# Performance work log

Hardware: AMD Instinct MI355X
Metric: run time of the kernel (lower is better)

The kernel has to match this reference:

```python
import jax, jax.numpy as jnp
import numpy as np
import math

S = 8192
D = 1024


def setup_inputs() -> dict:
    key = jax.random.key(0)
    kq, kk, kv = jax.random.split(key, 3)
    q = jax.random.normal(kq, (S, D), dtype=jnp.float32)
    k = jax.random.normal(kk, (S, D), dtype=jnp.float32)
    v = jax.random.normal(kv, (S, D), dtype=jnp.float32)
    return {"q": q, "k": k, "v": v}


def reference(q, k, v):
    # att[s_q, s_k] = q . k  (contract over d), scaled by 1/sqrt(d_model)
    d_model = q.shape[-1]
    scale = 1.0 / math.sqrt(d_model)
    att = jnp.einsum('qd,kd->qk', q, k) * scale
    # Original module applies its manual max-stable softmax over dim=1,
    # which for this rank-2 score matrix is the key axis (last axis).
    att_score = jax.nn.softmax(att, axis=1)
    return jnp.einsum('qk,kd->qd', att_score, v)
```

## Files before the change

### kernel.cpp

```cpp
#include <hip/hip_runtime.h>
#include <hip/hip_bf16.h>

#define S 8192
#define D 1024
#define QBLK 32
#define NW 8
#define KVBLK 256
#define NITER (S/KVBLK)
#define NTHR (NW*64)

typedef short short8 __attribute__((ext_vector_type(8)));
typedef float f32x16 __attribute__((ext_vector_type(16)));

__device__ __forceinline__ unsigned short f2bf(float x) {
    unsigned u = __builtin_bit_cast(unsigned, x);
    u += 0x7FFFu + ((u >> 16) & 1u);
    return (unsigned short)(u >> 16);
}
__device__ __forceinline__ float fexp2(float x) { return __builtin_amdgcn_exp2f(x); }

__device__ __forceinline__ short8 lds_r16(const char* rowbase, int off, int swz) {
    uint2 a = *(const uint2*)(rowbase + (off ^ swz));
    uint2 b = *(const uint2*)(rowbase + ((off + 8) ^ swz));
    int4 w; w.x = (int)a.x; w.y = (int)a.y; w.z = (int)b.x; w.w = (int)b.y;
    return __builtin_bit_cast(short8, w);
}
__device__ __forceinline__ void lds_w16(char* rowbase, int off, int swz, short8 v) {
    int4 w = __builtin_bit_cast(int4, v);
    uint2 a; a.x = (unsigned)w.x; a.y = (unsigned)w.y;
    uint2 b; b.x = (unsigned)w.z; b.y = (unsigned)w.w;
    *(uint2*)(rowbase + (off ^ swz))       = a;
    *(uint2*)(rowbase + ((off + 8) ^ swz)) = b;
}

__global__ void pack_k_kernel(const float* __restrict__ in, unsigned short* __restrict__ out) {
    int idx  = blockIdx.x * 256 + threadIdx.x;
    int lane = idx & 63, dc = (idx >> 6) & 63, kt = idx >> 12;
    int row = kt * 32 + (lane & 31), col = dc * 16 + (lane >> 5) * 8;
    const float4* p = (const float4*)(in + (size_t)row * D + col);
    float4 a = p[0], b = p[1];
    short8 v;
    v[0] = (short)f2bf(a.x); v[1] = (short)f2bf(a.y); v[2] = (short)f2bf(a.z); v[3] = (short)f2bf(a.w);
    v[4] = (short)f2bf(b.x); v[5] = (short)f2bf(b.y); v[6] = (short)f2bf(b.z); v[7] = (short)f2bf(b.w);
    *(short8*)(out + (size_t)idx * 8) = v;
}

__global__ void pack_v_kernel(const float* __restrict__ in, unsigned short* __restrict__ out) {
    int idx  = blockIdx.x * 256 + threadIdx.x;
    int lane = idx & 63, db = (idx >> 6) & 31, kc = (idx >> 11) & 15, t = idx >> 15;
    int col = db * 32 + (lane & 31);
    int rowbase = t * 256 + kc * 16 + (lane >> 5) * 8;
    short8 v;
#pragma unroll
    for (int j = 0; j < 8; ++j)
        v[j] = (short)f2bf(in[(size_t)(rowbase + j) * D + col]);
    *(short8*)(out + (size_t)idx * 8) = v;
}

template<bool CONV>
__global__ __launch_bounds__(NTHR, 2)
void attn_kernel(const float* __restrict__ Qf,
                 const unsigned short* __restrict__ Kpk,
                 const unsigned short* __restrict__ Vpk,
                 const float* __restrict__ Kf,
                 const float* __restrict__ Vf,
                 float* __restrict__ Out)
{
    __shared__ unsigned short q_lds[QBLK * D];
    __shared__ unsigned short p_lds[QBLK * KVBLK];
    __shared__ float red_m[NW][QBLK];
    __shared__ float red_l[NW][QBLK];
    __shared__ float alpha_sh[QBLK];
    __shared__ float invl_sh[QBLK];

    const int tid  = threadIdx.x;
    const int wid  = tid >> 6;
    const int lane = tid & 63;
    const int ln31 = lane & 31;
    const int hi   = (lane >> 5) & 1;
    const int q0   = blockIdx.x * QBLK;
    const int swz  = (ln31 & 15) << 3;

    {
        const float cscale = 1.44269504088896340736f / 32.0f;
        const float* qg = Qf + (size_t)q0 * D;
        char* qb = (char*)q_lds;
#pragma unroll
        for (int it = 0; it < (QBLK * D) / (NTHR * 8); ++it) {
            int idx = (it * NTHR + tid) * 8;
            int qq = idx >> 10, dd = idx & (D - 1);
            const float4* p4 = (const float4*)(qg + idx);
            float4 a = p4[0], b = p4[1];
            short8 v;
            v[0] = (short)f2bf(a.x * cscale); v[1] = (short)f2bf(a.y * cscale);
            v[2] = (short)f2bf(a.z * cscale); v[3] = (short)f2bf(a.w * cscale);
            v[4] = (short)f2bf(b.x * cscale); v[5] = (short)f2bf(b.y * cscale);
            v[6] = (short)f2bf(b.z * cscale); v[7] = (short)f2bf(b.w * cscale);
            lds_w16(qb + qq * 2048, dd * 2, (qq & 15) << 3, v);
        }
    }

    f32x16 O0, O1, O2, O3;
#pragma unroll
    for (int i = 0; i < 16; ++i) { O0[i] = 0.f; O1[i] = 0.f; O2[i] = 0.f; O3[i] = 0.f; }
    float m_run = -1e30f, l_run = 0.f;

    __syncthreads();

    for (int t = 0; t < NITER; ++t) {
        f32x16 s0, s1;
#pragma unroll
        for (int i = 0; i < 16; ++i) { s0[i] = 0.f; s1[i] = 0.f; }

        const char* qb = (const char*)q_lds + ln31 * 2048;
        __builtin_amdgcn_s_setprio(1);
        if (CONV) {
            const unsigned short* kg = Kpk + ((size_t)(t * 8 + wid) * 4096 + lane) * 8;
#pragma unroll 8
            for (int dc = 0; dc < 64; dc += 2) {
                short8 a0 = *(const short8*)(kg + (size_t)dc * 512);
                short8 b0 = lds_r16(qb, dc * 32 + hi * 16, swz);
                s0 = __builtin_amdgcn_mfma_f32_32x32x16_bf16(a0, b0, s0, 0, 0, 0);
                short8 a1 = *(const short8*)(kg + (size_t)(dc + 1) * 512);
                short8 b1 = lds_r16(qb, (dc + 1) * 32 + hi * 16, swz);
                s1 = __builtin_amdgcn_mfma_f32_32x32x16_bf16(a1, b1, s1, 0, 0, 0);
            }
        } else {
            const int krow = t * KVBLK + wid * 32 + ln31;
            const float* kg = Kf + (size_t)krow * D + hi * 8;
#pragma unroll 2
            for (int dc = 0; dc < 64; ++dc) {
                const float4* f4 = (const float4*)(kg + dc * 16);
                float4 x = f4[0], y = f4[1];
                short8 a0;
                a0[0] = (short)f2bf(x.x); a0[1] = (short)f2bf(x.y); a0[2] = (short)f2bf(x.z); a0[3] = (short)f2bf(x.w);
                a0[4] = (short)f2bf(y.x); a0[5] = (short)f2bf(y.y); a0[6] = (short)f2bf(y.z); a0[7] = (short)f2bf(y.w);
                short8 b0 = lds_r16(qb, dc * 32 + hi * 16, swz);
                s0 = __builtin_amdgcn_mfma_f32_32x32x16_bf16(a0, b0, s0, 0, 0, 0);
            }
        }
        __builtin_amdgcn_s_setprio(0);
#pragma unroll
        for (int i = 0; i < 16; ++i) s0[i] += s1[i];

        float mloc = s0[0];
#pragma unroll
        for (int r = 1; r < 16; ++r) mloc = fmaxf(mloc, s0[r]);
        mloc = fmaxf(mloc, __shfl_xor(mloc, 32));
        if (lane < 32) red_m[wid][ln31] = mloc;
        __syncthreads();

        float mt = red_m[0][ln31];
#pragma unroll
        for (int w = 1; w < NW; ++w) mt = fmaxf(mt, red_m[w][ln31]);
        float mnew  = fmaxf(m_run, mt);
        float alpha = fexp2(m_run - mnew);

        float pr[16];
        float lloc = 0.f;
#pragma unroll
        for (int r = 0; r < 16; ++r) { pr[r] = fexp2(s0[r] - mnew); lloc += pr[r]; }
        lloc += __shfl_xor(lloc, 32);
        if (lane < 32) { red_l[wid][ln31] = lloc; if (wid == 0) alpha_sh[ln31] = alpha; }

        {
            char* pb = (char*)p_lds + ln31 * 512;
#pragma unroll
            for (int g = 0; g < 4; ++g) {
                unsigned p01 = (unsigned)f2bf(pr[4 * g + 0]) | ((unsigned)f2bf(pr[4 * g + 1]) << 16);
                unsigned p23 = (unsigned)f2bf(pr[4 * g + 2]) | ((unsigned)f2bf(pr[4 * g + 3]) << 16);
                uint2 val = make_uint2(p01, p23);
                int koff = (wid * 32 + 8 * g + 4 * hi) * 2;
                *(uint2*)(pb + (koff ^ swz)) = val;
            }
        }
        __syncthreads();

        float lsum = red_l[0][ln31];
#pragma unroll
        for (int w = 1; w < NW; ++w) lsum += red_l[w][ln31];
        l_run = l_run * alpha + lsum;
        m_run = mnew;

#pragma unroll
        for (int r = 0; r < 16; ++r) {
            float ar = alpha_sh[(r & 3) + 8 * (r >> 2) + 4 * hi];
            O0[r] *= ar; O1[r] *= ar; O2[r] *= ar; O3[r] *= ar;
        }

        const char* pbase = (const char*)p_lds + ln31 * 512;
        __builtin_amdgcn_s_setprio(1);
        if (CONV) {
            const unsigned short* vg = Vpk + ((size_t)(t * 16) * 2048 + (size_t)wid * 64 + lane) * 8;
#pragma unroll 4
            for (int kc = 0; kc < 16; ++kc) {
                short8 pa = lds_r16(pbase, kc * 32 + hi * 16, swz);
                const unsigned short* vk = vg + (size_t)kc * 16384;
                short8 v0 = *(const short8*)(vk);
                O0 = __builtin_amdgcn_mfma_f32_32x32x16_bf16(pa, v0, O0, 0, 0, 0);
                short8 v1 = *(const short8*)(vk + 4096);
                O1 = __builtin_amdgcn_mfma_f32_32x32x16_bf16(pa, v1, O1, 0, 0, 0);
                short8 v2 = *(const short8*)(vk + 8192);
                O2 = __builtin_amdgcn_mfma_f32_32x32x16_bf16(pa, v2, O2, 0, 0, 0);
                short8 v3 = *(const short8*)(vk + 12288);
                O3 = __builtin_amdgcn_mfma_f32_32x32x16_bf16(pa, v3, O3, 0, 0, 0);
            }
        } else {
            const int dcol0 = wid * 32 + ln31;
#pragma unroll 2
            for (int kc = 0; kc < 16; ++kc) {
                short8 pa = lds_r16(pbase, kc * 32 + hi * 16, swz);
                const float* vf = Vf + (size_t)(t * 256 + kc * 16 + hi * 8) * D + dcol0;
#pragma unroll
                for (int f = 0; f < 4; ++f) {
                    short8 vb;
#pragma unroll
                    for (int j = 0; j < 8; ++j)
                        vb[j] = (short)f2bf(vf[(size_t)j * D + f * 256]);
                    if (f == 0) O0 = __builtin_amdgcn_mfma_f32_32x32x16_bf16(pa, vb, O0, 0, 0, 0);
                    if (f == 1) O1 = __builtin_amdgcn_mfma_f32_32x32x16_bf16(pa, vb, O1, 0, 0, 0);
                    if (f == 2) O2 = __builtin_amdgcn_mfma_f32_32x32x16_bf16(pa, vb, O2, 0, 0, 0);
                    if (f == 3) O3 = __builtin_amdgcn_mfma_f32_32x32x16_bf16(pa, vb, O3, 0, 0, 0);
                }
            }
        }
        __builtin_amdgcn_s_setprio(0);
    }

    if (wid == 0 && lane < 32) invl_sh[ln31] = 1.0f / l_run;
    __syncthreads();

    float* outp = Out + (size_t)q0 * D + wid * 32 + ln31;
#pragma unroll
    for (int r = 0; r < 16; ++r) {
        int qrow = (r & 3) + 8 * (r >> 2) + 4 * hi;
        float inv = invl_sh[qrow];
        outp[(size_t)qrow * D + 0]   = O0[r] * inv;
        outp[(size_t)qrow * D + 256] = O1[r] * inv;
        outp[(size_t)qrow * D + 512] = O2[r] * inv;
        outp[(size_t)qrow * D + 768] = O3[r] * inv;
    }
}

extern "C" void kernel_launch(void* const* d_in, const int* in_sizes, int n_in,
                              void* d_out, int out_size, void* d_ws, size_t ws_size,
                              hipStream_t stream)
{
    const float* q = (const float*)d_in[0];
    const float* k = (const float*)d_in[1];
    const float* v = (const float*)d_in[2];
    float* out = (float*)d_out;

    const size_t need = (size_t)2 * S * D * sizeof(unsigned short);
    if (ws_size >= need) {
        unsigned short* kpk = (unsigned short*)d_ws;
        unsigned short* vpk = kpk + (size_t)S * D;
        hipLaunchKernelGGL(pack_k_kernel, dim3(S * D / (256 * 8)), dim3(256), 0, stream, k, kpk);
        hipLaunchKernelGGL(pack_v_kernel, dim3(S * D / (256 * 8)), dim3(256), 0, stream, v, vpk);
        hipLaunchKernelGGL((attn_kernel<true>), dim3(S / QBLK), dim3(NTHR), 0, stream,
                           q, kpk, vpk, (const float*)nullptr, (const float*)nullptr, out);
    } else {
        hipLaunchKernelGGL((attn_kernel<false>), dim3(S / QBLK), dim3(NTHR), 0, stream,
                           q, (const unsigned short*)nullptr, (const unsigned short*)nullptr, k, v, out);
    }
}
```

Measured before the change: 633.5 us.

## Software-pipeline QK^T of next tile with PV of current tile

```diff
diff --git a/kernel.cpp b/kernel.cpp
--- a/kernel.cpp
+++ b/kernel.cpp
@@ -57,17 +57,53 @@
     *(short8*)(out + (size_t)idx * 8) = v;
 }
 
-template<bool CONV>
+#define SOFTMAX_PHASE(BUF)                                                        \
+    {                                                                             \
+        _Pragma("unroll")                                                         \
+        for (int i = 0; i < 16; ++i) s0[i] += s1[i];                              \
+        float mloc = s0[0];                                                       \
+        _Pragma("unroll")                                                         \
+        for (int r = 1; r < 16; ++r) mloc = fmaxf(mloc, s0[r]);                   \
+        mloc = fmaxf(mloc, __shfl_xor(mloc, 32));                                 \
+        if (lane < 32) red_m[wid][ln31] = mloc;                                   \
+        __syncthreads();                                                          \
+        float mt = red_m[0][ln31];                                                \
+        _Pragma("unroll")                                                         \
+        for (int w = 1; w < NW; ++w) mt = fmaxf(mt, red_m[w][ln31]);              \
+        float mnew  = fmaxf(m_run, mt);                                           \
+        float alpha = fexp2(m_run - mnew);                                        \
+        float pr[16]; float lloc = 0.f;                                           \
+        _Pragma("unroll")                                                         \
+        for (int r = 0; r < 16; ++r) { pr[r] = fexp2(s0[r] - mnew); lloc += pr[r]; } \
+        lloc += __shfl_xor(lloc, 32);                                             \
+        if (lane < 32) { red_l[wid][ln31] = lloc; if (wid == 0) alpha_sh[ln31] = alpha; } \
+        {                                                                         \
+            char* pb = (char*)(&p_lds[BUF][0]) + ln31 * 512;                      \
+            _Pragma("unroll")                                                     \
+            for (int g = 0; g < 4; ++g) {                                         \
+                unsigned p01 = (unsigned)f2bf(pr[4*g+0]) | ((unsigned)f2bf(pr[4*g+1]) << 16); \
+                unsigned p23 = (unsigned)f2bf(pr[4*g+2]) | ((unsigned)f2bf(pr[4*g+3]) << 16); \
+                uint2 val = make_uint2(p01, p23);                                 \
+                int koff = (wid * 32 + 8 * g + 4 * hi) * 2;                       \
+                *(uint2*)(pb + (koff ^ swz)) = val;                               \
+            }                                                                     \
+        }                                                                         \
+        __syncthreads();                                                          \
+        float lsum = red_l[0][ln31];                                              \
+        _Pragma("unroll")                                                         \
+        for (int w = 1; w < NW; ++w) lsum += red_l[w][ln31];                      \
+        l_run = l_run * alpha + lsum;                                             \
+        m_run = mnew;                                                             \
+    }
+
 __global__ __launch_bounds__(NTHR, 2)
-void attn_kernel(const float* __restrict__ Qf,
-                 const unsigned short* __restrict__ Kpk,
-                 const unsigned short* __restrict__ Vpk,
-                 const float* __restrict__ Kf,
-                 const float* __restrict__ Vf,
-                 float* __restrict__ Out)
+void attn_pipe_kernel(const float* __restrict__ Qf,
+                      const unsigned short* __restrict__ Kpk,
+                      const unsigned short* __restrict__ Vpk,
+                      float* __restrict__ Out)
 {
     __shared__ unsigned short q_lds[QBLK * D];
-    __shared__ unsigned short p_lds[QBLK * KVBLK];
+    __shared__ unsigned short p_lds[2][QBLK * KVBLK];
     __shared__ float red_m[NW][QBLK];
     __shared__ float red_l[NW][QBLK];
     __shared__ float alpha_sh[QBLK];
@@ -84,7 +120,7 @@
     {
         const float cscale = 1.44269504088896340736f / 32.0f;
         const float* qg = Qf + (size_t)q0 * D;
-        char* qb = (char*)q_lds;
+        char* qbw = (char*)q_lds;
 #pragma unroll
         for (int it = 0; it < (QBLK * D) / (NTHR * 8); ++it) {
             int idx = (it * NTHR + tid) * 8;
@@ -96,135 +132,189 @@
             v[2] = (short)f2bf(a.z * cscale); v[3] = (short)f2bf(a.w * cscale);
             v[4] = (short)f2bf(b.x * cscale); v[5] = (short)f2bf(b.y * cscale);
             v[6] = (short)f2bf(b.z * cscale); v[7] = (short)f2bf(b.w * cscale);
-            lds_w16(qb + qq * 2048, dd * 2, (qq & 15) << 3, v);
-        }
-    }
-
-    f32x16 O0, O1, O2, O3;
+            lds_w16(qbw + qq * 2048, dd * 2, (qq & 15) << 3, v);
+        }
+    }
+
+    f32x16 O0, O1, O2, O3, s0, s1;
 #pragma unroll
     for (int i = 0; i < 16; ++i) { O0[i] = 0.f; O1[i] = 0.f; O2[i] = 0.f; O3[i] = 0.f; }
     float m_run = -1e30f, l_run = 0.f;
 
     __syncthreads();
 
+    const char* qb = (const char*)q_lds + ln31 * 2048;
+
+    {
+#pragma unroll
+        for (int i = 0; i < 16; ++i) { s0[i] = 0.f; s1[i] = 0.f; }
+        const unsigned short* kg = Kpk + ((size_t)(0 * 8 + wid) * 4096 + lane) * 8;
+        __builtin_amdgcn_s_setprio(1);
+#pragma unroll 8
+        for (int dc = 0; dc < 64; dc += 2) {
+            short8 a0 = *(const short8*)(kg + (size_t)dc * 512);
+            short8 b0 = lds_r16(qb, dc * 32 + hi * 16, swz);
+            s0 = __builtin_amdgcn_mfma_f32_32x32x16_bf16(a0, b0, s0, 0, 0, 0);
+            short8 a1 = *(const short8*)(kg + (size_t)(dc + 1) * 512);
+            short8 b1 = lds_r16(qb, (dc + 1) * 32 + hi * 16, swz);
+            s1 = __builtin_amdgcn_mfma_f32_32x32x16_bf16(a1, b1, s1, 0, 0, 0);
+        }
+        __builtin_amdgcn_s_setprio(0);
+    }
+    SOFTMAX_PHASE(0)
+
+    int cur = 0;
     for (int t = 0; t < NITER; ++t) {
-        f32x16 s0, s1;
-#pragma unroll
-        for (int i = 0; i < 16; ++i) { s0[i] = 0.f; s1[i] = 0.f; }
-
-        const char* qb = (const char*)q_lds + ln31 * 2048;
-        __builtin_amdgcn_s_setprio(1);
-        if (CONV) {
-            const unsigned short* kg = Kpk + ((size_t)(t * 8 + wid) * 4096 + lane) * 8;
-#pragma unroll 8
-            for (int dc = 0; dc < 64; dc += 2) {
-                short8 a0 = *(const short8*)(kg + (size_t)dc * 512);
-                short8 b0 = lds_r16(qb, dc * 32 + hi * 16, swz);
-                s0 = __builtin_amdgcn_mfma_f32_32x32x16_bf16(a0, b0, s0, 0, 0, 0);
-                short8 a1 = *(const short8*)(kg + (size_t)(dc + 1) * 512);
-                short8 b1 = lds_r16(qb, (dc + 1) * 32 + hi * 16, swz);
-                s1 = __builtin_amdgcn_mfma_f32_32x32x16_bf16(a1, b1, s1, 0, 0, 0);
-            }
-        } else {
-            const int krow = t * KVBLK + wid * 32 + ln31;
-            const float* kg = Kf + (size_t)krow * D + hi * 8;
-#pragma unroll 2
-            for (int dc = 0; dc < 64; ++dc) {
-                const float4* f4 = (const float4*)(kg + dc * 16);
-                float4 x = f4[0], y = f4[1];
-                short8 a0;
-                a0[0] = (short)f2bf(x.x); a0[1] = (short)f2bf(x.y); a0[2] = (short)f2bf(x.z); a0[3] = (short)f2bf(x.w);
-                a0[4] = (short)f2bf(y.x); a0[5] = (short)f2bf(y.y); a0[6] = (short)f2bf(y.z); a0[7] = (short)f2bf(y.w);
-                short8 b0 = lds_r16(qb, dc * 32 + hi * 16, swz);
-                s0 = __builtin_amdgcn_mfma_f32_32x32x16_bf16(a0, b0, s0, 0, 0, 0);
-            }
-        }
-        __builtin_amdgcn_s_setprio(0);
-#pragma unroll
-        for (int i = 0; i < 16; ++i) s0[i] += s1[i];
-
-        float mloc = s0[0];
-#pragma unroll
-        for (int r = 1; r < 16; ++r) mloc = fmaxf(mloc, s0[r]);
-        mloc = fmaxf(mloc, __shfl_xor(mloc, 32));
-        if (lane < 32) red_m[wid][ln31] = mloc;
-        __syncthreads();
-
-        float mt = red_m[0][ln31];
-#pragma unroll
-        for (int w = 1; w < NW; ++w) mt = fmaxf(mt, red_m[w][ln31]);
-        float mnew  = fmaxf(m_run, mt);
-        float alpha = fexp2(m_run - mnew);
-
-        float pr[16];
-        float lloc = 0.f;
-#pragma unroll
-        for (int r = 0; r < 16; ++r) { pr[r] = fexp2(s0[r] - mnew); lloc += pr[r]; }
-        lloc += __shfl_xor(lloc, 32);
-        if (lane < 32) { red_l[wid][ln31] = lloc; if (wid == 0) alpha_sh[ln31] = alpha; }
-
-        {
-            char* pb = (char*)p_lds + ln31 * 512;
-#pragma unroll
-            for (int g = 0; g < 4; ++g) {
-                unsigned p01 = (unsigned)f2bf(pr[4 * g + 0]) | ((unsigned)f2bf(pr[4 * g + 1]) << 16);
-                unsigned p23 = (unsigned)f2bf(pr[4 * g + 2]) | ((unsigned)f2bf(pr[4 * g + 3]) << 16);
-                uint2 val = make_uint2(p01, p23);
-                int koff = (wid * 32 + 8 * g + 4 * hi) * 2;
-                *(uint2*)(pb + (koff ^ swz)) = val;
-            }
-        }
-        __syncthreads();
-
-        float lsum = red_l[0][ln31];
-#pragma unroll
-        for (int w = 1; w < NW; ++w) lsum += red_l[w][ln31];
-        l_run = l_run * alpha + lsum;
-        m_run = mnew;
-
 #pragma unroll
         for (int r = 0; r < 16; ++r) {
             float ar = alpha_sh[(r & 3) + 8 * (r >> 2) + 4 * hi];
             O0[r] *= ar; O1[r] *= ar; O2[r] *= ar; O3[r] *= ar;
         }
-
-        const char* pbase = (const char*)p_lds + ln31 * 512;
+        const char* pbase = (const char*)(&p_lds[cur][0]) + ln31 * 512;
+        const unsigned short* vg = Vpk + ((size_t)(t * 16) * 2048 + (size_t)wid * 64 + lane) * 8;
+
         __builtin_amdgcn_s_setprio(1);
-        if (CONV) {
-            const unsigned short* vg = Vpk + ((size_t)(t * 16) * 2048 + (size_t)wid * 64 + lane) * 8;
+        if (t + 1 < NITER) {
+#pragma unroll
+            for (int i = 0; i < 16; ++i) { s0[i] = 0.f; s1[i] = 0.f; }
+            const unsigned short* kg = Kpk + ((size_t)((t + 1) * 8 + wid) * 4096 + lane) * 8;
+            short8 pa{};
+#pragma unroll 8
+            for (int i = 0; i < 64; ++i) {
+                const int kc = i >> 2, f = i & 3;
+                if (f == 0) pa = lds_r16(pbase, kc * 32 + hi * 16, swz);
+                short8 ak = *(const short8*)(kg + (size_t)i * 512);
+                short8 bq = lds_r16(qb, i * 32 + hi * 16, swz);
+                if (i & 1) s1 = __builtin_amdgcn_mfma_f32_32x32x16_bf16(ak, bq, s1, 0, 0, 0);
+                else       s0 = __builtin_amdgcn_mfma_f32_32x32x16_bf16(ak, bq, s0, 0, 0, 0);
+                short8 vv = *(const short8*)(vg + (size_t)kc * 16384 + (size_t)f * 4096);
+                if      (f == 0) O0 = __builtin_amdgcn_mfma_f32_32x32x16_bf16(pa, vv, O0, 0, 0, 0);
+                else if (f == 1) O1 = __builtin_amdgcn_mfma_f32_32x32x16_bf16(pa, vv, O1, 0, 0, 0);
+                else if (f == 2) O2 = __builtin_amdgcn_mfma_f32_32x32x16_bf16(pa, vv, O2, 0, 0, 0);
+                else             O3 = __builtin_amdgcn_mfma_f32_32x32x16_bf16(pa, vv, O3, 0, 0, 0);
+            }
+        } else {
 #pragma unroll 4
             for (int kc = 0; kc < 16; ++kc) {
                 short8 pa = lds_r16(pbase, kc * 32 + hi * 16, swz);
                 const unsigned short* vk = vg + (size_t)kc * 16384;
-                short8 v0 = *(const short8*)(vk);
-                O0 = __builtin_amdgcn_mfma_f32_32x32x16_bf16(pa, v0, O0, 0, 0, 0);
-                short8 v1 = *(const short8*)(vk + 4096);
-                O1 = __builtin_amdgcn_mfma_f32_32x32x16_bf16(pa, v1, O1, 0, 0, 0);
-                short8 v2 = *(const short8*)(vk + 8192);
-                O2 = __builtin_amdgcn_mfma_f32_32x32x16_bf16(pa, v2, O2, 0, 0, 0);
-                short8 v3 = *(const short8*)(vk + 12288);
-                O3 = __builtin_amdgcn_mfma_f32_32x32x16_bf16(pa, v3, O3, 0, 0, 0);
+                O0 = __builtin_amdgcn_mfma_f32_32x32x16_bf16(pa, *(const short8*)(vk),         O0, 0, 0, 0);
+                O1 = __builtin_amdgcn_mfma_f32_32x32x16_bf16(pa, *(const short8*)(vk + 4096),  O1, 0, 0, 0);
+                O2 = __builtin_amdgcn_mfma_f32_32x32x16_bf16(pa, *(const short8*)(vk + 8192),  O2, 0, 0, 0);
+                O3 = __builtin_amdgcn_mfma_f32_32x32x16_bf16(pa, *(const short8*)(vk + 12288), O3, 0, 0, 0);
             }
-        } else {
-            const int dcol0 = wid * 32 + ln31;
+        }
+        __builtin_amdgcn_s_setprio(0);
+
+        if (t + 1 < NITER) {
+            if (cur == 0) { SOFTMAX_PHASE(1) } else { SOFTMAX_PHASE(0) }
+        }
+        cur ^= 1;
+    }
+
+    if (wid == 0 && lane < 32) invl_sh[ln31] = 1.0f / l_run;
+    __syncthreads();
+
+    float* outp = Out + (size_t)q0 * D + wid * 32 + ln31;
+#pragma unroll
+    for (int r = 0; r < 16; ++r) {
+        int qrow = (r & 3) + 8 * (r >> 2) + 4 * hi;
+        float inv = invl_sh[qrow];
+        outp[(size_t)qrow * D + 0]   = O0[r] * inv;
+        outp[(size_t)qrow * D + 256] = O1[r] * inv;
+        outp[(size_t)qrow * D + 512] = O2[r] * inv;
+        outp[(size_t)qrow * D + 768] = O3[r] * inv;
+    }
+}
+
+__global__ __launch_bounds__(NTHR, 2)
+void attn_fallback_kernel(const float* __restrict__ Qf,
+                          const float* __restrict__ Kf,
+                          const float* __restrict__ Vf,
+                          float* __restrict__ Out)
+{
+    __shared__ unsigned short q_lds[QBLK * D];
+    __shared__ unsigned short p_lds[1][QBLK * KVBLK];
+    __shared__ float red_m[NW][QBLK];
+    __shared__ float red_l[NW][QBLK];
+    __shared__ float alpha_sh[QBLK];
+    __shared__ float invl_sh[QBLK];
+
+    const int tid  = threadIdx.x;
+    const int wid  = tid >> 6;
+    const int lane = tid & 63;
+    const int ln31 = lane & 31;
+    const int hi   = (lane >> 5) & 1;
+    const int q0   = blockIdx.x * QBLK;
+    const int swz  = (ln31 & 15) << 3;
+
+    {
+        const float cscale = 1.44269504088896340736f / 32.0f;
+        const float* qg = Qf + (size_t)q0 * D;
+        char* qbw = (char*)q_lds;
+#pragma unroll
+        for (int it = 0; it < (QBLK * D) / (NTHR * 8); ++it) {
+            int idx = (it * NTHR + tid) * 8;
+            int qq = idx >> 10, dd = idx & (D - 1);
+            const float4* p4 = (const float4*)(qg + idx);
+            float4 a = p4[0], b = p4[1];
+            short8 v;
+            v[0] = (short)f2bf(a.x * cscale); v[1] = (short)f2bf(a.y * cscale);
+            v[2] = (short)f2bf(a.z * cscale); v[3] = (short)f2bf(a.w * cscale);
+            v[4] = (short)f2bf(b.x * cscale); v[5] = (short)f2bf(b.y * cscale);
+            v[6] = (short)f2bf(b.z * cscale); v[7] = (short)f2bf(b.w * cscale);
+            lds_w16(qbw + qq * 2048, dd * 2, (qq & 15) << 3, v);
+        }
+    }
+
+    f32x16 O0, O1, O2, O3, s0, s1;
+#pragma unroll
+    for (int i = 0; i < 16; ++i) { O0[i] = 0.f; O1[i] = 0.f; O2[i] = 0.f; O3[i] = 0.f; }
+    float m_run = -1e30f, l_run = 0.f;
+
+    __syncthreads();
+    const char* qb = (const char*)q_lds + ln31 * 2048;
+
+    for (int t = 0; t < NITER; ++t) {
+#pragma unroll
+        for (int i = 0; i < 16; ++i) { s0[i] = 0.f; s1[i] = 0.f; }
+        const int krow = t * KVBLK + wid * 32 + ln31;
+        const float* kg = Kf + (size_t)krow * D + hi * 8;
 #pragma unroll 2
-            for (int kc = 0; kc < 16; ++kc) {
-                short8 pa = lds_r16(pbase, kc * 32 + hi * 16, swz);
-                const float* vf = Vf + (size_t)(t * 256 + kc * 16 + hi * 8) * D + dcol0;
-#pragma unroll
-                for (int f = 0; f < 4; ++f) {
-                    short8 vb;
-#pragma unroll
-                    for (int j = 0; j < 8; ++j)
-                        vb[j] = (short)f2bf(vf[(size_t)j * D + f * 256]);
-                    if (f == 0) O0 = __builtin_amdgcn_mfma_f32_32x32x16_bf16(pa, vb, O0, 0, 0, 0);
-                    if (f == 1) O1 = __builtin_amdgcn_mfma_f32_32x32x16_bf16(pa, vb, O1, 0, 0, 0);
-                    if (f == 2) O2 = __builtin_amdgcn_mfma_f32_32x32x16_bf16(pa, vb, O2, 0, 0, 0);
-                    if (f == 3) O3 = __builtin_amdgcn_mfma_f32_32x32x16_bf16(pa, vb, O3, 0, 0, 0);
-                }
+        for (int dc = 0; dc < 64; ++dc) {
+            const float4* f4 = (const float4*)(kg + dc * 16);
+            float4 x = f4[0], y = f4[1];
+            short8 a0;
+            a0[0] = (short)f2bf(x.x); a0[1] = (short)f2bf(x.y); a0[2] = (short)f2bf(x.z); a0[3] = (short)f2bf(x.w);
+            a0[4] = (short)f2bf(y.x); a0[5] = (short)f2bf(y.y); a0[6] = (short)f2bf(y.z); a0[7] = (short)f2bf(y.w);
+            short8 b0 = lds_r16(qb, dc * 32 + hi * 16, swz);
+            s0 = __builtin_amdgcn_mfma_f32_32x32x16_bf16(a0, b0, s0, 0, 0, 0);
+        }
+        SOFTMAX_PHASE(0)
+#pragma unroll
+        for (int r = 0; r < 16; ++r) {
+            float ar = alpha_sh[(r & 3) + 8 * (r >> 2) + 4 * hi];
+            O0[r] *= ar; O1[r] *= ar; O2[r] *= ar; O3[r] *= ar;
+        }
+        const char* pbase = (const char*)(&p_lds[0][0]) + ln31 * 512;
+        const int dcol0 = wid * 32 + ln31;
+#pragma unroll 2
+        for (int kc = 0; kc < 16; ++kc) {
+            short8 pa = lds_r16(pbase, kc * 32 + hi * 16, swz);
+            const float* vf = Vf + (size_t)(t * 256 + kc * 16 + hi * 8) * D + dcol0;
+#pragma unroll
+            for (int f = 0; f < 4; ++f) {
+                short8 vb;
+#pragma unroll
+                for (int j = 0; j < 8; ++j)
+                    vb[j] = (short)f2bf(vf[(size_t)j * D + f * 256]);
+                if (f == 0) O0 = __builtin_amdgcn_mfma_f32_32x32x16_bf16(pa, vb, O0, 0, 0, 0);
+                if (f == 1) O1 = __builtin_amdgcn_mfma_f32_32x32x16_bf16(pa, vb, O1, 0, 0, 0);
+                if (f == 2) O2 = __builtin_amdgcn_mfma_f32_32x32x16_bf16(pa, vb, O2, 0, 0, 0);
+                if (f == 3) O3 = __builtin_amdgcn_mfma_f32_32x32x16_bf16(pa, vb, O3, 0, 0, 0);
             }
         }
-        __builtin_amdgcn_s_setprio(0);
+        __syncthreads();
     }
 
     if (wid == 0 && lane < 32) invl_sh[ln31] = 1.0f / l_run;
@@ -257,10 +347,10 @@
         unsigned short* vpk = kpk + (size_t)S * D;
         hipLaunchKernelGGL(pack_k_kernel, dim3(S * D / (256 * 8)), dim3(256), 0, stream, k, kpk);
         hipLaunchKernelGGL(pack_v_kernel, dim3(S * D / (256 * 8)), dim3(256), 0, stream, v, vpk);
-        hipLaunchKernelGGL((attn_kernel<true>), dim3(S / QBLK), dim3(NTHR), 0, stream,
-                           q, kpk, vpk, (const float*)nullptr, (const float*)nullptr, out);
+        hipLaunchKernelGGL(attn_pipe_kernel, dim3(S / QBLK), dim3(NTHR), 0, stream,
+                           q, kpk, vpk, out);
     } else {
-        hipLaunchKernelGGL((attn_kernel<false>), dim3(S / QBLK), dim3(NTHR), 0, stream,
-                           q, (const unsigned short*)nullptr, (const unsigned short*)nullptr, k, v, out);
-    }
-}
+        hipLaunchKernelGGL(attn_fallback_kernel, dim3(S / QBLK), dim3(NTHR), 0, stream,
+                           q, k, v, out);
+    }
+}
```

After: 836.2 us. 1.32x slower.
